# Kernel optimization log

Hardware: AMD Instinct MI355X
Metric: run time of the kernel (lower is better)

## Reference

```python
import jax, jax.numpy as jnp
import numpy as np

N_STEPS = 10
DT = 0.01
TAU = 0.1
LAM = 0.1


def setup_inputs() -> dict:
    key = jax.random.key(0)
    k1, k2 = jax.random.split(key)
    x = jax.random.normal(k1, (4, 2048, 1024), dtype=jnp.float32)
    W = jax.random.normal(k2, (1024, 4096), dtype=jnp.float32) * 0.02
    return {"x": x, "W": W}


def reference(x, W):
    orig_shape = x.shape
    D = orig_shape[-1]
    x_flat = x.reshape(-1, D)                      # [N, d_model]
    b = x_flat @ W                                 # [N, d_lca]
    G = W.T @ W                                    # [d_lca, d_lca]
    G = G - jnp.diag(jnp.diag(G))                  # zero self-inhibition
    u0 = jnp.zeros_like(b)

    def step(u, _):
        a = jax.nn.relu(u - LAM)
        du = (b - a @ G - u) / TAU
        return u + DT * du, None

    u, _ = jax.lax.scan(step, u0, None, length=N_STEPS)
    a = jax.nn.relu(u - LAM)
    out = a @ W.T                                  # [N, d_model]
    return out.reshape(orig_shape)
```

## Files before the change

kernel.cpp:

```cpp
#include <hip/hip_runtime.h>
#include <hip/hip_bf16.h>


typedef __bf16 bf16_t;
typedef __bf16 bf16x8 __attribute__((ext_vector_type(8)));
typedef __bf16 bf16x4 __attribute__((ext_vector_type(4)));
typedef float  f32x4  __attribute__((ext_vector_type(4)));

__device__ __forceinline__ void g2lds16(const void* g, void* l) {
    __builtin_amdgcn_global_load_lds(
        (const __attribute__((address_space(1))) void*)g,
        (__attribute__((address_space(3))) void*)l,
        16, 0, 0);
}

template<int N> __device__ __forceinline__ void waitv() {
    if constexpr (N == 0) asm volatile("s_waitcnt vmcnt(0)" ::: "memory");
    else if constexpr (N == 1) asm volatile("s_waitcnt vmcnt(1)" ::: "memory");
    else if constexpr (N == 2) asm volatile("s_waitcnt vmcnt(2)" ::: "memory");
    else if constexpr (N == 3) asm volatile("s_waitcnt vmcnt(3)" ::: "memory");
    else if constexpr (N == 4) asm volatile("s_waitcnt vmcnt(4)" ::: "memory");
    else if constexpr (N == 5) asm volatile("s_waitcnt vmcnt(5)" ::: "memory");
    else if constexpr (N == 6) asm volatile("s_waitcnt vmcnt(6)" ::: "memory");
}
__device__ __forceinline__ void bar() { __builtin_amdgcn_s_barrier(); }
__device__ __forceinline__ void waitlgkm0() {
    asm volatile("s_waitcnt lgkmcnt(0)" ::: "memory");
}

template<int n> struct IC { static constexpr int v = n; };

enum { MODE_B = 0, MODE_T = 1, MODE_STEP2 = 2, MODE_OUT = 3 };

template<int MODE, int BM>
__global__ __launch_bounds__(512, 2)
void gemm_bt(const bf16_t* __restrict__ A, const bf16_t* __restrict__ Bt,
             int N, int K,
             float*  __restrict__ outF,
             bf16_t* __restrict__ outH,
             bf16_t* __restrict__ bb,
             bf16_t* __restrict__ u,
             const float* __restrict__ g)
{
    constexpr int BN  = 256;
    constexpr int FM  = BM / 32;
    constexpr int FMH = FM / 2;
    constexpr int ASZ = BM * 128;
    constexpr int BSZ = BN * 128;

    __shared__ __attribute__((aligned(16))) bf16_t As[(BM == 256 ? 2 : 1) * BM * 64];
    __shared__ __attribute__((aligned(16))) bf16_t Bs[2 * BN * 64];

    const int t = threadIdx.x;
    const int l = t & 63;
    const int w = t >> 6;
    const int wm = (w >> 2) * (BM / 4);
    const int wn = (w & 3) * 32;

    const int gx  = gridDim.x;
    const int nwg = gx * gridDim.y;
    const int bid = blockIdx.y * gx + blockIdx.x;
    const int sw  = (bid & 7) * (nwg >> 3) + (bid >> 3);
    const int rowA = (sw / gx) * BM;
    const int colB = (sw % gx) * BN;

    const int srow = t >> 3;
    const int scol = (((t & 7) ^ (srow & 7)) << 3);
    const bf16_t* gB = Bt + (size_t)(colB + srow) * K + scol;
    char* sB = (char*)Bs + t * 16;
    auto stB = [&](int slot, int kt, int uu) {
        g2lds16(gB + (size_t)uu * 64 * K + kt * 64, sB + slot * BSZ + uu * 8192);
    };

    const int lrow = l & 15;
    const int c0 = ((l >> 4) << 4) ^ ((l & 7) << 4);
    const char* cAs = (const char*)As;
    const char* cBs = (const char*)Bs;
    auto rdA = [&](int slot, int qi, int ii, int p) {
        return (const bf16x8*)(cAs + slot * ASZ
            + (size_t)(qi * (BM / 2) + wm + ii * 16 + lrow) * 128 + (c0 ^ (p << 6)));
    };
    auto rdB = [&](int slot, int qj, int jj, int p) {
        return (const bf16x8*)(cBs + slot * BSZ
            + (size_t)(qj * 128 + wn + jj * 16 + lrow) * 128 + (c0 ^ (p << 6)));
    };

    f32x4 acc[FM][4];
#pragma unroll
    for (int i = 0; i < FM; ++i)
#pragma unroll
        for (int j = 0; j < 4; ++j)
#pragma unroll
            for (int r = 0; r < 4; ++r) acc[i][j][r] = 0.f;

    const int NT = K >> 6;

    if constexpr (BM == 256) {
        const bf16_t* gA = A + (size_t)(rowA + srow) * K + scol;
        char* sA = (char*)As + t * 16;
        auto stA = [&](int slot, int kt, int uu) {
            g2lds16(gA + (size_t)uu * 64 * K + kt * 64, sA + slot * ASZ + uu * 8192);
        };

        auto tile = [&](auto W0, auto W1, auto W2, int slot, int ktN, bool st) {
            const int ns = slot ^ 1;
            bf16x8 af[FMH][2], bf0[2][2], bf1[2][2];
            if (st) { stB(ns, ktN, 0); stB(ns, ktN, 1); }
            waitv<decltype(W0)::v>(); bar();
#pragma unroll
            for (int ii = 0; ii < FMH; ++ii)
#pragma unroll
                for (int p = 0; p < 2; ++p) af[ii][p] = *rdA(slot, 0, ii, p);
#pragma unroll
            for (int jj = 0; jj < 2; ++jj)
#pragma unroll
                for (int p = 0; p < 2; ++p) bf0[jj][p] = *rdB(slot, 0, jj, p);
            __builtin_amdgcn_s_setprio(1);
#pragma unroll
            for (int ii = 0; ii < FMH; ++ii)
#pragma unroll
                for (int jj = 0; jj < 2; ++jj)
#pragma unroll
                    for (int p = 0; p < 2; ++p)
                        acc[ii][jj] = __builtin_amdgcn_mfma_f32_16x16x32_bf16(
                            bf0[jj][p], af[ii][p], acc[ii][jj], 0, 0, 0);
            __builtin_amdgcn_s_setprio(0);
            if (st) { stA(ns, ktN, 0); stA(ns, ktN, 1); }
            waitv<decltype(W1)::v>(); bar();
#pragma unroll
            for (int jj = 0; jj < 2; ++jj)
#pragma unroll
                for (int p = 0; p < 2; ++p) bf1[jj][p] = *rdB(slot, 1, jj, p);
            __builtin_amdgcn_s_setprio(1);
#pragma unroll
            for (int ii = 0; ii < FMH; ++ii)
#pragma unroll
                for (int jj = 0; jj < 2; ++jj)
#pragma unroll
                    for (int p = 0; p < 2; ++p)
                        acc[ii][2 + jj] = __builtin_amdgcn_mfma_f32_16x16x32_bf16(
                            bf1[jj][p], af[ii][p], acc[ii][2 + jj], 0, 0, 0);
            __builtin_amdgcn_s_setprio(0);
            if (st) { stB(ns, ktN, 2); stB(ns, ktN, 3); }
            waitv<decltype(W2)::v>(); bar();
#pragma unroll
            for (int ii = 0; ii < FMH; ++ii)
#pragma unroll
                for (int p = 0; p < 2; ++p) af[ii][p] = *rdA(slot, 1, ii, p);
            __builtin_amdgcn_s_setprio(1);
#pragma unroll
            for (int ii = 0; ii < FMH; ++ii)
#pragma unroll
                for (int jj = 0; jj < 2; ++jj)
#pragma unroll
                    for (int p = 0; p < 2; ++p)
                        acc[FMH + ii][2 + jj] = __builtin_amdgcn_mfma_f32_16x16x32_bf16(
                            bf1[jj][p], af[ii][p], acc[FMH + ii][2 + jj], 0, 0, 0);
            __builtin_amdgcn_s_setprio(0);
            if (st) { stA(ns, ktN, 2); stA(ns, ktN, 3); }
            __builtin_amdgcn_s_setprio(1);
#pragma unroll
            for (int ii = 0; ii < FMH; ++ii)
#pragma unroll
                for (int jj = 0; jj < 2; ++jj)
#pragma unroll
                    for (int p = 0; p < 2; ++p)
                        acc[FMH + ii][jj] = __builtin_amdgcn_mfma_f32_16x16x32_bf16(
                            bf0[jj][p], af[ii][p], acc[FMH + ii][jj], 0, 0, 0);
            __builtin_amdgcn_s_setprio(0);
        };

        stB(0, 0, 0); stB(0, 0, 1);
        stA(0, 0, 0); stA(0, 0, 1);
        stB(0, 0, 2); stB(0, 0, 3);
        stA(0, 0, 2); stA(0, 0, 3);

        for (int kt = 0; kt < NT - 1; ++kt)
            tile(IC<6>{}, IC<6>{}, IC<6>{}, kt & 1, kt + 1, true);
        tile(IC<4>{}, IC<2>{}, IC<0>{}, (NT - 1) & 1, 0, false);
    } else {
        const int s_arow = t >> 3;
        const int s_acb  = ((t & 7) << 4) ^ ((s_arow & 7) << 4);
        const bf16_t* gAr = A + (size_t)(rowA + s_arow) * K + (t & 7) * 8;
        auto reluv = [&](bf16x8 v) {
            bf16x8 r;
#pragma unroll
            for (int e = 0; e < 8; ++e)
                r[e] = (bf16_t)fmaxf((float)v[e] - 0.1f, 0.f);
            return r;
        };
        auto wrA = [&](bf16x8 v, int gg) {
            *(bf16x8*)((char*)As + (size_t)(gg * 64 + s_arow) * 128 + s_acb) = v;
        };

        {
            bf16x8 a0 = *(const bf16x8*)(gAr);
            bf16x8 a1 = *(const bf16x8*)(gAr + (size_t)64 * K);
            waitv<0>();
            wrA(reluv(a0), 0);
            wrA(reluv(a1), 1);
            waitlgkm0();
            stB(0, 0, 0); stB(0, 0, 1); stB(0, 0, 2); stB(0, 0, 3);
        }

        for (int kt = 0; kt < NT; ++kt) {
            const bool st = (kt + 1 < NT);
            const int slot = kt & 1, ns = slot ^ 1;
            bf16x8 af[FMH][2], bf0[2][2], bf1[2][2];
            bf16x8 nA0, nA1;
            if (st) {
                nA0 = *(const bf16x8*)(gAr + (kt + 1) * 64);
                nA1 = *(const bf16x8*)(gAr + (size_t)64 * K + (kt + 1) * 64);
            }
            if (st) waitv<4>(); else waitv<2>();
            bar();
#pragma unroll
            for (int ii = 0; ii < FMH; ++ii)
#pragma unroll
                for (int p = 0; p < 2; ++p) af[ii][p] = *rdA(0, 0, ii, p);
#pragma unroll
            for (int jj = 0; jj < 2; ++jj)
#pragma unroll
                for (int p = 0; p < 2; ++p) bf0[jj][p] = *rdB(slot, 0, jj, p);
            __builtin_amdgcn_s_setprio(1);
#pragma unroll
            for (int ii = 0; ii < FMH; ++ii)
#pragma unroll
                for (int jj = 0; jj < 2; ++jj)
#pragma unroll
                    for (int p = 0; p < 2; ++p)
                        acc[ii][jj] = __builtin_amdgcn_mfma_f32_16x16x32_bf16(
                            bf0[jj][p], af[ii][p], acc[ii][jj], 0, 0, 0);
            __builtin_amdgcn_s_setprio(0);
            if (st) { stB(ns, kt + 1, 0); stB(ns, kt + 1, 1); }
            if (st) waitv<4>(); else waitv<0>();
            bar();
#pragma unroll
            for (int jj = 0; jj < 2; ++jj)
#pragma unroll
                for (int p = 0; p < 2; ++p) bf1[jj][p] = *rdB(slot, 1, jj, p);
            __builtin_amdgcn_s_setprio(1);
#pragma unroll
            for (int ii = 0; ii < FMH; ++ii)
#pragma unroll
                for (int jj = 0; jj < 2; ++jj)
#pragma unroll
                    for (int p = 0; p < 2; ++p)
                        acc[ii][2 + jj] = __builtin_amdgcn_mfma_f32_16x16x32_bf16(
                            bf1[jj][p], af[ii][p], acc[ii][2 + jj], 0, 0, 0);
            __builtin_amdgcn_s_setprio(0);
            if (st) { stB(ns, kt + 1, 2); stB(ns, kt + 1, 3); }
#pragma unroll
            for (int ii = 0; ii < FMH; ++ii)
#pragma unroll
                for (int p = 0; p < 2; ++p) af[ii][p] = *rdA(0, 1, ii, p);
            __builtin_amdgcn_s_setprio(1);
#pragma unroll
            for (int ii = 0; ii < FMH; ++ii)
#pragma unroll
                for (int jj = 0; jj < 2; ++jj)
#pragma unroll
                    for (int p = 0; p < 2; ++p)
                        acc[FMH + ii][2 + jj] = __builtin_amdgcn_mfma_f32_16x16x32_bf16(
                            bf1[jj][p], af[ii][p], acc[FMH + ii][2 + jj], 0, 0, 0);
            __builtin_amdgcn_s_setprio(0);
            bar();
            if (st) {
                waitv<4>();
                wrA(reluv(nA0), 0);
                wrA(reluv(nA1), 1);
                waitlgkm0();
            }
            __builtin_amdgcn_s_setprio(1);
#pragma unroll
            for (int ii = 0; ii < FMH; ++ii)
#pragma unroll
                for (int jj = 0; jj < 2; ++jj)
#pragma unroll
                    for (int p = 0; p < 2; ++p)
                        acc[FMH + ii][jj] = __builtin_amdgcn_mfma_f32_16x16x32_bf16(
                            bf0[jj][p], af[ii][p], acc[FMH + ii][jj], 0, 0, 0);
            __builtin_amdgcn_s_setprio(0);
        }
    }

    const int m0 = rowA + wm + lrow;
    const int n0 = colB + wn + ((l >> 4) * 4);

    f32x4 gvv[4];
    if constexpr (MODE == MODE_STEP2) {
#pragma unroll
        for (int j = 0; j < 4; ++j)
            gvv[j] = *(const f32x4*)(g + n0 + (j & 1) * 16 + (j >> 1) * 128);
    }

#pragma unroll
    for (int i = 0; i < FM; ++i) {
        const int m = m0 + (i & (FMH - 1)) * 16 + (i / FMH) * (BM / 2);
#pragma unroll
        for (int j = 0; j < 4; ++j) {
            const size_t idx = (size_t)m * N + (n0 + (j & 1) * 16 + (j >> 1) * 128);
            const f32x4 c = acc[i][j];
            if constexpr (MODE == MODE_T) {
                bf16x4 o;
#pragma unroll
                for (int r = 0; r < 4; ++r) o[r] = (bf16_t)c[r];
                *(bf16x4*)(outH + idx) = o;
            } else if constexpr (MODE == MODE_B) {
                bf16x4 ob, ou;
#pragma unroll
                for (int r = 0; r < 4; ++r) {
                    const float un = 0.1f * c[r];
                    ob[r] = (bf16_t)c[r];
                    ou[r] = (bf16_t)un;
                }
                *(bf16x4*)(bb + idx) = ob;
                *(bf16x4*)(u  + idx) = ou;
            } else if constexpr (MODE == MODE_STEP2) {
                const bf16x4 uv = *(const bf16x4*)(u  + idx);
                const bf16x4 bv = *(const bf16x4*)(bb + idx);
                bf16x4 ou;
#pragma unroll
                for (int r = 0; r < 4; ++r) {
                    const float uo = (float)uv[r];
                    const float ao = fmaxf(uo - 0.1f, 0.f);
                    const float un = 0.9f * uo + 0.1f * (float)bv[r]
                                   - 0.1f * c[r] + 0.1f * ao * gvv[j][r];
                    ou[r] = (bf16_t)un;
                }
                *(bf16x4*)(u + idx) = ou;
            } else {
                *(f32x4*)(outF + idx) = c;
            }
        }
    }
}

__global__ void cast_x_kernel(const float* __restrict__ x, bf16_t* __restrict__ xh, int n) {
    int i = blockIdx.x * 256 + threadIdx.x;
    if (i < n) xh[i] = (bf16_t)x[i];
}

__global__ void prep_w_kernel(const float* __restrict__ W,
                              bf16_t* __restrict__ Wh, bf16_t* __restrict__ WT) {
    int i = blockIdx.x * 256 + threadIdx.x;
    if (i < 1024 * 4096) {
        int k = i >> 12;
        int n = i & 4095;
        bf16_t v = (bf16_t)W[i];
        Wh[i] = v;
        WT[(size_t)n * 1024 + k] = v;
    }
}

__global__ void prep_g_kernel(const float* __restrict__ W, float* __restrict__ g) {
    int j = blockIdx.x * 256 + threadIdx.x;
    if (j < 4096) {
        float s = 0.f;
        for (int k = 0; k < 1024; ++k) {
            float v = W[(size_t)k * 4096 + j];
            s += v * v;
        }
        g[j] = s;
    }
}

extern "C" void kernel_launch(void* const* d_in, const int* in_sizes, int n_in,
                              void* d_out, int out_size, void* d_ws, size_t ws_size,
                              hipStream_t stream)
{
    const float* x = (const float*)d_in[0];
    const float* W = (const float*)d_in[1];

    bf16_t* xh = (bf16_t*)d_out;
    bf16_t* tt = (bf16_t*)d_out;
    float*  gd = (float*)((char*)d_out + 16777216);

    char* ws = (char*)d_ws;
    bf16_t* bb = (bf16_t*)(ws + 67108864);
    bf16_t* u  = (bf16_t*)(ws + 134217728);
    bf16_t* Wh = (bf16_t*)(ws + 201326592);
    bf16_t* WT = (bf16_t*)(ws + 209715200);

    cast_x_kernel<<<8388608 / 256, 256, 0, stream>>>(x, xh, 8388608);
    prep_w_kernel<<<4194304 / 256, 256, 0, stream>>>(W, Wh, WT);
    prep_g_kernel<<<16, 256, 0, stream>>>(W, gd);

    gemm_bt<MODE_B, 256><<<dim3(16, 32), 512, 0, stream>>>(xh, WT, 4096, 1024,
                                                           nullptr, nullptr, bb, u, nullptr);
    for (int s = 0; s < 9; ++s) {
        gemm_bt<MODE_T, 128><<<dim3(4, 64), 512, 0, stream>>>(u, Wh, 1024, 4096,
                                                              nullptr, tt, nullptr, nullptr, nullptr);
        gemm_bt<MODE_STEP2, 256><<<dim3(16, 32), 512, 0, stream>>>(tt, WT, 4096, 1024,
                                                                   nullptr, nullptr, bb, u, gd);
    }
    gemm_bt<MODE_OUT, 128><<<dim3(4, 64), 512, 0, stream>>>(u, Wh, 1024, 4096,
                                                            (float*)d_out, nullptr, nullptr, nullptr, nullptr);
}
```

Before: 2.037 ms.

## Double-buffer relu A tiles in step GEMM and speed up prep kernels

The relu-transformed A operand in the BM=128 GEMM path now goes through a double-buffered shared-memory tile. The next tile is prefetched two iterations ahead and written into the alternate slot during compute, which removes one barrier per k-step. The prep kernels are also reworked: the x cast is vectorized, the W transpose goes through a shared-memory tile for coalesced writes, and the g column-norm reduction is split across more blocks with atomics after a zeroing kernel. The cost is doubled A shared memory for BM=128, which may affect occupancy, plus an extra launch and atomics in setup.

```diff
diff --git a/kernel.cpp b/kernel.cpp
--- a/kernel.cpp
+++ b/kernel.cpp
@@ -27,6 +27,7 @@
 __device__ __forceinline__ void waitlgkm0() {
     asm volatile("s_waitcnt lgkmcnt(0)" ::: "memory");
 }
+__device__ __forceinline__ void fence() { asm volatile("" ::: "memory"); }
 
 template<int n> struct IC { static constexpr int v = n; };
 
@@ -48,7 +49,7 @@
     constexpr int ASZ = BM * 128;
     constexpr int BSZ = BN * 128;
 
-    __shared__ __attribute__((aligned(16))) bf16_t As[(BM == 256 ? 2 : 1) * BM * 64];
+    __shared__ __attribute__((aligned(16))) bf16_t As[2 * BM * 64];
     __shared__ __attribute__((aligned(16))) bf16_t Bs[2 * BN * 64];
 
     const int t = threadIdx.x;
@@ -189,35 +190,41 @@
                 r[e] = (bf16_t)fmaxf((float)v[e] - 0.1f, 0.f);
             return r;
         };
-        auto wrA = [&](bf16x8 v, int gg) {
-            *(bf16x8*)((char*)As + (size_t)(gg * 64 + s_arow) * 128 + s_acb) = v;
+        auto wrA = [&](bf16x8 v, int gg, int slot) {
+            *(bf16x8*)((char*)As + slot * ASZ
+                       + (size_t)(gg * 64 + s_arow) * 128 + s_acb) = v;
         };
 
+        bf16x8 curA0, curA1;
         {
-            bf16x8 a0 = *(const bf16x8*)(gAr);
-            bf16x8 a1 = *(const bf16x8*)(gAr + (size_t)64 * K);
+            bf16x8 p0 = *(const bf16x8*)(gAr);
+            bf16x8 p1 = *(const bf16x8*)(gAr + (size_t)64 * K);
             waitv<0>();
-            wrA(reluv(a0), 0);
-            wrA(reluv(a1), 1);
+            wrA(reluv(p0), 0, 0);
+            wrA(reluv(p1), 1, 0);
             waitlgkm0();
+            curA0 = *(const bf16x8*)(gAr + 64);
+            curA1 = *(const bf16x8*)(gAr + (size_t)64 * K + 64);
+            fence();
             stB(0, 0, 0); stB(0, 0, 1); stB(0, 0, 2); stB(0, 0, 3);
         }
 
         for (int kt = 0; kt < NT; ++kt) {
-            const bool st = (kt + 1 < NT);
             const int slot = kt & 1, ns = slot ^ 1;
+            const bool iA = (kt + 2 < NT);
+            const bool sB = (kt + 1 < NT);
             bf16x8 af[FMH][2], bf0[2][2], bf1[2][2];
             bf16x8 nA0, nA1;
-            if (st) {
-                nA0 = *(const bf16x8*)(gAr + (kt + 1) * 64);
-                nA1 = *(const bf16x8*)(gAr + (size_t)64 * K + (kt + 1) * 64);
+            if (iA) {
+                nA0 = *(const bf16x8*)(gAr + (kt + 2) * 64);
+                nA1 = *(const bf16x8*)(gAr + (size_t)64 * K + (kt + 2) * 64);
             }
-            if (st) waitv<4>(); else waitv<2>();
+            if (kt < NT - 2) waitv<4>(); else waitv<2>();
             bar();
 #pragma unroll
             for (int ii = 0; ii < FMH; ++ii)
 #pragma unroll
-                for (int p = 0; p < 2; ++p) af[ii][p] = *rdA(0, 0, ii, p);
+                for (int p = 0; p < 2; ++p) af[ii][p] = *rdA(slot, 0, ii, p);
 #pragma unroll
             for (int jj = 0; jj < 2; ++jj)
 #pragma unroll
@@ -232,8 +239,10 @@
                         acc[ii][jj] = __builtin_amdgcn_mfma_f32_16x16x32_bf16(
                             bf0[jj][p], af[ii][p], acc[ii][jj], 0, 0, 0);
             __builtin_amdgcn_s_setprio(0);
-            if (st) { stB(ns, kt + 1, 0); stB(ns, kt + 1, 1); }
-            if (st) waitv<4>(); else waitv<0>();
+            if (sB) { stB(ns, kt + 1, 0); stB(ns, kt + 1, 1); }
+            if (kt < NT - 2) waitv<4>();
+            else if (kt == NT - 2) waitv<2>();
+            else waitv<0>();
             bar();
 #pragma unroll
             for (int jj = 0; jj < 2; ++jj)
@@ -249,11 +258,15 @@
                         acc[ii][2 + jj] = __builtin_amdgcn_mfma_f32_16x16x32_bf16(
                             bf1[jj][p], af[ii][p], acc[ii][2 + jj], 0, 0, 0);
             __builtin_amdgcn_s_setprio(0);
-            if (st) { stB(ns, kt + 1, 2); stB(ns, kt + 1, 3); }
-#pragma unroll
-            for (int ii = 0; ii < FMH; ++ii)
-#pragma unroll
-                for (int p = 0; p < 2; ++p) af[ii][p] = *rdA(0, 1, ii, p);
+            if (sB) { stB(ns, kt + 1, 2); stB(ns, kt + 1, 3); }
+#pragma unroll
+            for (int ii = 0; ii < FMH; ++ii)
+#pragma unroll
+                for (int p = 0; p < 2; ++p) af[ii][p] = *rdA(slot, 1, ii, p);
+            if (sB) {
+                wrA(reluv(curA0), 0, ns);
+                wrA(reluv(curA1), 1, ns);
+            }
             __builtin_amdgcn_s_setprio(1);
 #pragma unroll
             for (int ii = 0; ii < FMH; ++ii)
@@ -264,13 +277,7 @@
                         acc[FMH + ii][2 + jj] = __builtin_amdgcn_mfma_f32_16x16x32_bf16(
                             bf1[jj][p], af[ii][p], acc[FMH + ii][2 + jj], 0, 0, 0);
             __builtin_amdgcn_s_setprio(0);
-            bar();
-            if (st) {
-                waitv<4>();
-                wrA(reluv(nA0), 0);
-                wrA(reluv(nA1), 1);
-                waitlgkm0();
-            }
+            waitlgkm0();
             __builtin_amdgcn_s_setprio(1);
 #pragma unroll
             for (int ii = 0; ii < FMH; ++ii)
@@ -281,6 +288,7 @@
                         acc[FMH + ii][jj] = __builtin_amdgcn_mfma_f32_16x16x32_bf16(
                             bf0[jj][p], af[ii][p], acc[FMH + ii][jj], 0, 0, 0);
             __builtin_amdgcn_s_setprio(0);
+            if (iA) { curA0 = nA0; curA1 = nA1; }
         }
     }
 
@@ -337,32 +345,48 @@
 }
 
 __global__ void cast_x_kernel(const float* __restrict__ x, bf16_t* __restrict__ xh, int n) {
-    int i = blockIdx.x * 256 + threadIdx.x;
-    if (i < n) xh[i] = (bf16_t)x[i];
+    int i = (blockIdx.x * 256 + threadIdx.x) * 4;
+    if (i < n) {
+        f32x4 v = *(const f32x4*)(x + i);
+        bf16x4 o;
+#pragma unroll
+        for (int r = 0; r < 4; ++r) o[r] = (bf16_t)v[r];
+        *(bf16x4*)(xh + i) = o;
+    }
 }
 
 __global__ void prep_w_kernel(const float* __restrict__ W,
                               bf16_t* __restrict__ Wh, bf16_t* __restrict__ WT) {
+    __shared__ bf16_t tile[64][130];
+    const int k0 = blockIdx.y * 64;
+    const int n0 = blockIdx.x * 128;
+    for (int e = threadIdx.x; e < 64 * 128; e += 256) {
+        const int kk = e >> 7, nn = e & 127;
+        const bf16_t v = (bf16_t)W[(size_t)(k0 + kk) * 4096 + n0 + nn];
+        Wh[(size_t)(k0 + kk) * 4096 + n0 + nn] = v;
+        tile[kk][nn] = v;
+    }
+    __syncthreads();
+    for (int e = threadIdx.x; e < 64 * 128; e += 256) {
+        const int nn = e >> 6, kk = e & 63;
+        WT[(size_t)(n0 + nn) * 1024 + k0 + kk] = tile[kk][nn];
+    }
+}
+
+__global__ void zero_g_kernel(float* __restrict__ g) {
     int i = blockIdx.x * 256 + threadIdx.x;
-    if (i < 1024 * 4096) {
-        int k = i >> 12;
-        int n = i & 4095;
-        bf16_t v = (bf16_t)W[i];
-        Wh[i] = v;
-        WT[(size_t)n * 1024 + k] = v;
-    }
+    if (i < 4096) g[i] = 0.f;
 }
 
 __global__ void prep_g_kernel(const float* __restrict__ W, float* __restrict__ g) {
-    int j = blockIdx.x * 256 + threadIdx.x;
-    if (j < 4096) {
-        float s = 0.f;
-        for (int k = 0; k < 1024; ++k) {
-            float v = W[(size_t)k * 4096 + j];
-            s += v * v;
-        }
-        g[j] = s;
-    }
+    const int j  = blockIdx.x * 256 + threadIdx.x;
+    const int k0 = blockIdx.y * 128;
+    float s = 0.f;
+    for (int k = k0; k < k0 + 128; ++k) {
+        const float v = W[(size_t)k * 4096 + j];
+        s += v * v;
+    }
+    atomicAdd(g + j, s);
 }
 
 extern "C" void kernel_launch(void* const* d_in, const int* in_sizes, int n_in,
@@ -382,9 +406,10 @@
     bf16_t* Wh = (bf16_t*)(ws + 201326592);
     bf16_t* WT = (bf16_t*)(ws + 209715200);
 
-    cast_x_kernel<<<8388608 / 256, 256, 0, stream>>>(x, xh, 8388608);
-    prep_w_kernel<<<4194304 / 256, 256, 0, stream>>>(W, Wh, WT);
-    prep_g_kernel<<<16, 256, 0, stream>>>(W, gd);
+    cast_x_kernel<<<8388608 / 1024, 256, 0, stream>>>(x, xh, 8388608);
+    prep_w_kernel<<<dim3(32, 16), 256, 0, stream>>>(W, Wh, WT);
+    zero_g_kernel<<<16, 256, 0, stream>>>(gd);
+    prep_g_kernel<<<dim3(16, 8), 256, 0, stream>>>(W, gd);
 
     gemm_bt<MODE_B, 256><<<dim3(16, 32), 512, 0, stream>>>(xh, WT, 4096, 1024,
                                                            nullptr, nullptr, bb, u, nullptr);
```

Result: faster. 1.775 ms (-12.9%).
